# Optimization experiments

Hardware: AMD Instinct MI355X
Metric: run time of the kernel (lower is better)

The kernel has to match this reference:

```python
import jax, jax.numpy as jnp
import numpy as np

N, E, D = 100000, 1600000, 128
EPS = 1e-5


def _bn(h, g, b):
    m = h.mean(0)
    v = ((h - m) ** 2).mean(0)  # biased var, as torch BatchNorm1d normalization
    return g * (h - m) / jnp.sqrt(v + EPS) + b


def _sage(x, src, dst, w_self, w_neigh, b, n):
    # mean aggregation over in-neighbors (edges src->dst)
    agg = jax.ops.segment_sum(x[src], dst, num_segments=n)          # [N, D]
    cnt = jax.ops.segment_sum(jnp.ones(src.shape, x.dtype), dst, num_segments=n)
    mean = agg / jnp.maximum(cnt, 1.0)[:, None]
    return x @ w_self + mean @ w_neigh + b


def setup_inputs() -> dict:
    key = jax.random.key(0)
    ks = jax.random.split(key, 8)
    s = 1.0 / np.sqrt(D)
    return {
        "x": jax.random.normal(ks[0], (N, D), jnp.float32),
        "src": jax.random.randint(ks[1], (E,), 0, N, jnp.int32),
        "dst": jax.random.randint(ks[2], (E,), 0, N, jnp.int32),
        "w_self1": jax.random.normal(ks[3], (D, D), jnp.float32) * s,
        "w_neigh1": jax.random.normal(ks[4], (D, D), jnp.float32) * s,
        "b1": jnp.zeros((D,), jnp.float32),
        "w_self2": jax.random.normal(ks[5], (D, D), jnp.float32) * s,
        "w_neigh2": jax.random.normal(ks[6], (D, D), jnp.float32) * s,
        "b2": jnp.zeros((D,), jnp.float32),
        "w_skip": jax.random.normal(ks[7], (D, D), jnp.float32) * s,
        "b_skip": jnp.zeros((D,), jnp.float32),
        "g1": jnp.ones((D,), jnp.float32), "be1": jnp.zeros((D,), jnp.float32),
        "g2": jnp.ones((D,), jnp.float32), "be2": jnp.zeros((D,), jnp.float32),
        "g3": jnp.ones((D,), jnp.float32), "be3": jnp.zeros((D,), jnp.float32),
    }


def reference(x, src, dst, w_self1, w_neigh1, b1, w_self2, w_neigh2, b2,
              w_skip, b_skip, g1, be1, g2, be2, g3, be3):
    n = x.shape[0]
    h1 = _sage(x, src, dst, w_self1, w_neigh1, b1, n)
    h1 = jax.nn.relu(_bn(h1, g1, be1))           # dropout: eval-mode identity
    h2 = _sage(h1, src, dst, w_self2, w_neigh2, b2, n)
    h2 = _bn(h2, g2, be2)
    skip = _bn(h1 @ w_skip + b_skip, g3, be3)
    return jax.nn.relu(h2 + skip)
```

## Files before the change

kernel.cpp:

```cpp
#include <hip/hip_runtime.h>

#define D 128
#define PCHUNK 4096
#define SCAP 8192

typedef short bf16x8 __attribute__((ext_vector_type(8)));
typedef float f32x4 __attribute__((ext_vector_type(4)));

__device__ __forceinline__ ushort f2b(float f){
  unsigned u = __builtin_bit_cast(unsigned, f);
  u += 0x7fffu + ((u >> 16) & 1u);
  return (ushort)(u >> 16);
}
__device__ __forceinline__ float b2f(ushort h){
  unsigned u = ((unsigned)h) << 16;
  return __builtin_bit_cast(float, u);
}

__global__ __launch_bounds__(256) void k_p0(const int* __restrict__ dst,
                                            int* __restrict__ bcnt, int E){
  __shared__ int h[512];
  for (int u=threadIdx.x; u<512; u+=256) h[u]=0;
  __syncthreads();
  for (long long i=(long long)blockIdx.x*256+threadIdx.x; i<E; i+=(long long)gridDim.x*256)
    atomicAdd(&h[dst[i]>>8], 1);
  __syncthreads();
  for (int u=threadIdx.x; u<512; u+=256) if (h[u]) atomicAdd(&bcnt[u], h[u]);
}

__global__ void k_bscan(const int* __restrict__ bcnt, int* __restrict__ bbase,
                        int* __restrict__ bcur, int nb, int E){
  __shared__ int sh[1024];
  int t = threadIdx.x;
  int v = (t<nb) ? bcnt[t] : 0;
  sh[t]=v; __syncthreads();
  for (int off=1; off<1024; off<<=1){
    int add = (t>=off)?sh[t-off]:0;
    __syncthreads();
    sh[t]+=add;
    __syncthreads();
  }
  if (t<nb){ int e=sh[t]-v; bbase[t]=e; bcur[t]=e; }
  if (t==nb) bbase[t]=E;
}

__global__ __launch_bounds__(256) void k_part(const int* __restrict__ src,
        const int* __restrict__ dst, int* __restrict__ bcur,
        int2* __restrict__ pairs, int E){
  __shared__ int hist[512], offA[512], offB[512], gbase[512];
  __shared__ int sS[PCHUNK], sD[PCHUNK];
  const int t = threadIdx.x;
  const int base = blockIdx.x * PCHUNK;
  const int cnt = min(PCHUNK, E - base);
  for (int u=t; u<512; u+=256) hist[u]=0;
  __syncthreads();
  int rs[16], rd[16];
  #pragma unroll
  for (int j=0;j<16;j++){
    int li = j*256 + t;
    if (li < cnt){
      rs[j]=src[base+li]; rd[j]=dst[base+li];
      atomicAdd(&hist[rd[j]>>8],1);
    } else { rs[j]=0; rd[j]=-1; }
  }
  __syncthreads();
  int *cur=offA, *nxt=offB;
  for (int u=t; u<512; u+=256) cur[u]=hist[u];
  __syncthreads();
  for (int off=1; off<512; off<<=1){
    for (int u=t; u<512; u+=256) nxt[u] = cur[u] + ((u>=off)?cur[u-off]:0);
    __syncthreads();
    int* tmp=cur; cur=nxt; nxt=tmp;
  }
  for (int u=t; u<512; u+=256) nxt[u] = cur[u]-hist[u];
  __syncthreads();
  #pragma unroll
  for (int j=0;j<16;j++){
    if (j*256+t < cnt){
      int b = rd[j]>>8;
      int p = atomicAdd(&nxt[b],1);
      sS[p]=rs[j]; sD[p]=rd[j];
    }
  }
  __syncthreads();
  for (int u=t; u<512; u+=256){
    int c = hist[u];
    if (c>0) gbase[u] = atomicAdd(&bcur[u], c);
  }
  __syncthreads();
  #pragma unroll
  for (int j=0;j<16;j++){
    int idx = j*256+t;
    if (idx<cnt){
      int d = sD[idx]; int b = d>>8;
      int gpos = gbase[b] + (idx - (cur[b]-hist[b]));
      pairs[gpos] = make_int2(sS[idx], d);
    }
  }
}

__global__ __launch_bounds__(256) void k_sortb(const int2* __restrict__ pairs,
        const int* __restrict__ bbase, int* __restrict__ offs,
        int* __restrict__ slots, int N, int NB){
  __shared__ int nh[256], nc[256], sc[256];
  __shared__ int stage[SCAP];
  const int b = blockIdx.x, t = threadIdx.x;
  const int base = bbase[b];
  const int cnt  = bbase[b+1] - base;
  nh[t]=0; __syncthreads();
  for (int i=t;i<cnt;i+=256) atomicAdd(&nh[pairs[base+i].y & 255],1);
  __syncthreads();
  int v = nh[t];
  sc[t]=v; __syncthreads();
  for (int off=1; off<256; off<<=1){
    int add = (t>=off)?sc[t-off]:0;
    __syncthreads();
    sc[t]+=add;
    __syncthreads();
  }
  int excl = sc[t]-v;
  nc[t]=excl;
  int node = (b<<8)+t;
  if (node<N) offs[node]=base+excl;
  if (b==NB-1 && t==0) offs[N]=bbase[NB];
  __syncthreads();
  if (cnt<=SCAP){
    for (int i=t;i<cnt;i+=256){
      int2 p = pairs[base+i];
      int pos = atomicAdd(&nc[p.y & 255],1);
      stage[pos]=p.x;
    }
    __syncthreads();
    for (int i=t;i<cnt;i+=256) slots[base+i]=stage[i];
  } else {
    for (int i=t;i<cnt;i+=256){
      int2 p = pairs[base+i];
      int pos = atomicAdd(&nc[p.y & 255],1);
      slots[base+pos]=p.x;
    }
  }
}

__global__ __launch_bounds__(256) void k_xcast(const float* __restrict__ x,
                                               ushort* __restrict__ xb, long long n4){
  long long i = (long long)blockIdx.x*256 + threadIdx.x;
  const long long stride = (long long)gridDim.x*256;
  for (; i < n4; i += stride){
    float4 v = reinterpret_cast<const float4*>(x)[i];
    ushort4 o;
    o.x = f2b(v.x); o.y = f2b(v.y); o.z = f2b(v.z); o.w = f2b(v.w);
    reinterpret_cast<ushort4*>(xb)[i] = o;
  }
}

__global__ void k_wt(const float* __restrict__ W, ushort* __restrict__ Wb, int K, int k0){
  int idx = blockIdx.x*256 + threadIdx.x;
  int k = idx >> 7, c = idx & 127;
  Wb[(size_t)c*K + k0 + k] = f2b(W[idx]);
}

__global__ __launch_bounds__(256) void k_gatherb(const ushort* __restrict__ Xb,
        const int* __restrict__ slots, const int* __restrict__ offs,
        ushort* __restrict__ meanb, int N){
  int node = blockIdx.x*4 + (threadIdx.x >> 6);
  int c2 = (threadIdx.x & 63) * 2;
  if (node >= N) return;
  const int beg = offs[node], end = offs[node+1];
  float sx0=0,sy0=0,sx1=0,sy1=0,sx2=0,sy2=0,sx3=0,sy3=0;
  int j = beg;
  while (j < end && (j & 3)){
    unsigned u = *reinterpret_cast<const unsigned*>(&Xb[(size_t)slots[j]*D + c2]);
    sx0 += b2f((ushort)u); sy0 += b2f((ushort)(u>>16));
    ++j;
  }
  const int nfull = (end - j) >> 2;
  const int4* sp = reinterpret_cast<const int4*>(slots + j);

#define G8(ia, ib) { \
    unsigned u0 = *reinterpret_cast<const unsigned*>(&Xb[(size_t)(ia).x*D + c2]); \
    unsigned u1 = *reinterpret_cast<const unsigned*>(&Xb[(size_t)(ia).y*D + c2]); \
    unsigned u2 = *reinterpret_cast<const unsigned*>(&Xb[(size_t)(ia).z*D + c2]); \
    unsigned u3 = *reinterpret_cast<const unsigned*>(&Xb[(size_t)(ia).w*D + c2]); \
    unsigned u4 = *reinterpret_cast<const unsigned*>(&Xb[(size_t)(ib).x*D + c2]); \
    unsigned u5 = *reinterpret_cast<const unsigned*>(&Xb[(size_t)(ib).y*D + c2]); \
    unsigned u6 = *reinterpret_cast<const unsigned*>(&Xb[(size_t)(ib).z*D + c2]); \
    unsigned u7 = *reinterpret_cast<const unsigned*>(&Xb[(size_t)(ib).w*D + c2]); \
    sx0 += b2f((ushort)u0); sy0 += b2f((ushort)(u0>>16)); \
    sx1 += b2f((ushort)u1); sy1 += b2f((ushort)(u1>>16)); \
    sx2 += b2f((ushort)u2); sy2 += b2f((ushort)(u2>>16)); \
    sx3 += b2f((ushort)u3); sy3 += b2f((ushort)(u3>>16)); \
    sx0 += b2f((ushort)u4); sy0 += b2f((ushort)(u4>>16)); \
    sx1 += b2f((ushort)u5); sy1 += b2f((ushort)(u5>>16)); \
    sx2 += b2f((ushort)u6); sy2 += b2f((ushort)(u6>>16)); \
    sx3 += b2f((ushort)u7); sy3 += b2f((ushort)(u7>>16)); }

  int g = 0;
  if (nfull >= 2){
    int4 ia = sp[0], ib = sp[1];
    for (g = 2; g + 2 <= nfull; g += 2){
      int4 na = sp[g], nb = sp[g+1];
      G8(ia, ib);
      ia = na; ib = nb;
    }
    G8(ia, ib);
  }
  if (g < nfull){
    int4 ia = sp[g];
    unsigned u0 = *reinterpret_cast<const unsigned*>(&Xb[(size_t)ia.x*D + c2]);
    unsigned u1 = *reinterpret_cast<const unsigned*>(&Xb[(size_t)ia.y*D + c2]);
    unsigned u2 = *reinterpret_cast<const unsigned*>(&Xb[(size_t)ia.z*D + c2]);
    unsigned u3 = *reinterpret_cast<const unsigned*>(&Xb[(size_t)ia.w*D + c2]);
    sx0 += b2f((ushort)u0); sy0 += b2f((ushort)(u0>>16));
    sx1 += b2f((ushort)u1); sy1 += b2f((ushort)(u1>>16));
    sx2 += b2f((ushort)u2); sy2 += b2f((ushort)(u2>>16));
    sx3 += b2f((ushort)u3); sy3 += b2f((ushort)(u3>>16));
  }
  j += 4*nfull;
  for (; j < end; ++j){
    unsigned u = *reinterpret_cast<const unsigned*>(&Xb[(size_t)slots[j]*D + c2]);
    sx0 += b2f((ushort)u); sy0 += b2f((ushort)(u>>16));
  }
#undef G8
  float deg = (float)(end - beg);
  float rc = deg > 0.f ? 1.0f/deg : 0.f;
  unsigned o = (unsigned)f2b((sx0+sx1+sx2+sx3)*rc)
             | ((unsigned)f2b((sy0+sy1+sy2+sy3)*rc) << 16);
  *reinterpret_cast<unsigned*>(&meanb[(size_t)node*D + c2]) = o;
}

template<bool SKIP>
__global__ __launch_bounds__(256, 2) void k_mfma(
    const ushort* __restrict__ A0, const ushort* __restrict__ A1,
    const ushort* __restrict__ Wb, const ushort* __restrict__ Wk,
    const float* __restrict__ bias, const float* __restrict__ biasK,
    ushort* __restrict__ C, ushort* __restrict__ Ck,
    float* __restrict__ gS, float* __restrict__ gQ,
    float* __restrict__ gSK, float* __restrict__ gQK, int N, int NT)
{
  __shared__ ushort At[2][64][40];
  __shared__ ushort Wt[2][128][40];
  __shared__ ushort Wkt[SKIP ? 2*128*40 : 1];
  __shared__ float shS[128], shQ[128], shSK[SKIP?128:1], shQK[SKIP?128:1];
  const int tid = threadIdx.x;
  if (tid < 128){ shS[tid]=0.f; shQ[tid]=0.f; if (SKIP){ shSK[tid]=0.f; shQK[tid]=0.f; } }
  const int bid = blockIdx.x, gridN = gridDim.x;
  const int lane = tid & 63, wid = tid >> 6;
  const int wr = wid >> 1, wc = wid & 1;
  const int lr = lane & 15, kq = lane >> 4;
  const int srA = tid >> 2, s8A = (tid & 3) * 8;
  const int srW = tid >> 2, s8W = (tid & 3) * 8;

  int4 va0, va1, va2, va3;
  int4 w0a,w0b, w1a,w1b, w2a,w2b, w3a,w3b;
  int4 k0a,k0b, k1a,k1b, k2a,k2b, k3a,k3b;

#define LOADSET(S, GT, TT) { \
    int grow_ = (GT)*64 + srA; if (grow_ >= N) grow_ = N-1; \
    const ushort* As_ = ((TT) >= 4) ? A1 : A0; \
    va##S = *reinterpret_cast<const int4*>(&As_[(size_t)grow_*D + ((TT)&3)*32 + s8A]); \
    w##S##a = *reinterpret_cast<const int4*>(&Wb[(size_t)srW*256 + (TT)*32 + s8W]); \
    w##S##b = *reinterpret_cast<const int4*>(&Wb[(size_t)(srW+64)*256 + (TT)*32 + s8W]); \
    if (SKIP && (TT) < 4){ \
      k##S##a = *reinterpret_cast<const int4*>(&Wk[(size_t)srW*128 + (TT)*32 + s8W]); \
      k##S##b = *reinterpret_cast<const int4*>(&Wk[(size_t)(srW+64)*128 + (TT)*32 + s8W]); \
    } }

#define WRITESET(S, BW, TT) { \
    *reinterpret_cast<int4*>(&At[BW][srA][s8A]) = va##S; \
    *reinterpret_cast<int4*>(&Wt[BW][srW][s8W]) = w##S##a; \
    *reinterpret_cast<int4*>(&Wt[BW][srW+64][s8W]) = w##S##b; \
    if (SKIP && (TT) < 4){ \
      *reinterpret_cast<int4*>(&Wkt[((BW)*128 + srW)*40 + s8W]) = k##S##a; \
      *reinterpret_cast<int4*>(&Wkt[((BW)*128 + srW + 64)*40 + s8W]) = k##S##b; \
    } }

#define PBAR() { asm volatile("s_waitcnt lgkmcnt(0)" ::: "memory"); \
    __builtin_amdgcn_s_barrier(); __builtin_amdgcn_sched_barrier(0); }

#define STEPBODY(BR, WITHK, ...) { \
    bf16x8 af0 = *reinterpret_cast<const bf16x8*>(&At[BR][32*wr + lr][kq*8]); \
    bf16x8 af1 = *reinterpret_cast<const bf16x8*>(&At[BR][32*wr + 16 + lr][kq*8]); \
    bf16x8 bw0 = *reinterpret_cast<const bf16x8*>(&Wt[BR][64*wc + lr][kq*8]); \
    bf16x8 bw1 = *reinterpret_cast<const bf16x8*>(&Wt[BR][64*wc + 16 + lr][kq*8]); \
    bf16x8 bw2 = *reinterpret_cast<const bf16x8*>(&Wt[BR][64*wc + 32 + lr][kq*8]); \
    bf16x8 bw3 = *reinterpret_cast<const bf16x8*>(&Wt[BR][64*wc + 48 + lr][kq*8]); \
    bf16x8 bk0{}, bk1{}, bk2{}, bk3{}; \
    if (SKIP && (WITHK)){ \
      bk0 = *reinterpret_cast<const bf16x8*>(&Wkt[((BR)*128 + 64*wc + lr)*40 + kq*8]); \
      bk1 = *reinterpret_cast<const bf16x8*>(&Wkt[((BR)*128 + 64*wc + 16 + lr)*40 + kq*8]); \
      bk2 = *reinterpret_cast<const bf16x8*>(&Wkt[((BR)*128 + 64*wc + 32 + lr)*40 + kq*8]); \
      bk3 = *reinterpret_cast<const bf16x8*>(&Wkt[((BR)*128 + 64*wc + 48 + lr)*40 + kq*8]); \
    } \
    __VA_ARGS__; \
    acc[0][0] = __builtin_amdgcn_mfma_f32_16x16x32_bf16(af0, bw0, acc[0][0], 0,0,0); \
    acc[0][1] = __builtin_amdgcn_mfma_f32_16x16x32_bf16(af0, bw1, acc[0][1], 0,0,0); \
    acc[0][2] = __builtin_amdgcn_mfma_f32_16x16x32_bf16(af0, bw2, acc[0][2], 0,0,0); \
    acc[0][3] = __builtin_amdgcn_mfma_f32_16x16x32_bf16(af0, bw3, acc[0][3], 0,0,0); \
    acc[1][0] = __builtin_amdgcn_mfma_f32_16x16x32_bf16(af1, bw0, acc[1][0], 0,0,0); \
    acc[1][1] = __builtin_amdgcn_mfma_f32_16x16x32_bf16(af1, bw1, acc[1][1], 0,0,0); \
    acc[1][2] = __builtin_amdgcn_mfma_f32_16x16x32_bf16(af1, bw2, acc[1][2], 0,0,0); \
    acc[1][3] = __builtin_amdgcn_mfma_f32_16x16x32_bf16(af1, bw3, acc[1][3], 0,0,0); \
    if (SKIP && (WITHK)){ \
      accK[0][0] = __builtin_amdgcn_mfma_f32_16x16x32_bf16(af0, bk0, accK[0][0], 0,0,0); \
      accK[0][1] = __builtin_amdgcn_mfma_f32_16x16x32_bf16(af0, bk1, accK[0][1], 0,0,0); \
      accK[0][2] = __builtin_amdgcn_mfma_f32_16x16x32_bf16(af0, bk2, accK[0][2], 0,0,0); \
      accK[0][3] = __builtin_amdgcn_mfma_f32_16x16x32_bf16(af0, bk3, accK[0][3], 0,0,0); \
      accK[1][0] = __builtin_amdgcn_mfma_f32_16x16x32_bf16(af1, bk0, accK[1][0], 0,0,0); \
      accK[1][1] = __builtin_amdgcn_mfma_f32_16x16x32_bf16(af1, bk1, accK[1][1], 0,0,0); \
      accK[1][2] = __builtin_amdgcn_mfma_f32_16x16x32_bf16(af1, bk2, accK[1][2], 0,0,0); \
      accK[1][3] = __builtin_amdgcn_mfma_f32_16x16x32_bf16(af1, bk3, accK[1][3], 0,0,0); \
    } }

  f32x4 acc[2][4], accK[SKIP?2:1][SKIP?4:1];
  #pragma unroll
  for (int m=0;m<2;m++)
    #pragma unroll
    for (int n=0;n<4;n++){
      acc[m][n] = (f32x4){0.f,0.f,0.f,0.f};
      if (SKIP) accK[m][n] = (f32x4){0.f,0.f,0.f,0.f};
    }
  float bs[4]={0,0,0,0}, bq[4]={0,0,0,0}, bsk[4]={0,0,0,0}, bqk[4]={0,0,0,0};
  float bv[4], bkv[4];
  #pragma unroll
  for (int n=0;n<4;n++){
    bv[n] = bias[64*wc + 16*n + lr];
    bkv[n] = SKIP ? biasK[64*wc + 16*n + lr] : 0.f;
  }

  {
    const int t0 = bid;
    LOADSET(0, t0, 0);
    LOADSET(1, t0, 1);
    LOADSET(2, t0, 2);
    LOADSET(3, t0, 3);
    WRITESET(0, 0, 0);
    PBAR();
  }

  for (int tile = bid; tile < NT; tile += gridN){
    const int tnext = tile + gridN;
    const bool hasnext = (tnext < NT);
    STEPBODY(0, 1, LOADSET(0, tile, 4));
    WRITESET(1, 1, 1); PBAR();
    STEPBODY(1, 1, LOADSET(1, tile, 5));
    WRITESET(2, 0, 2); PBAR();
    STEPBODY(0, 1, LOADSET(2, tile, 6));
    WRITESET(3, 1, 3); PBAR();
    STEPBODY(1, 1, LOADSET(3, tile, 7));
    WRITESET(0, 0, 4); PBAR();
    STEPBODY(0, 0, if (hasnext) LOADSET(0, tnext, 0));
    WRITESET(1, 1, 5); PBAR();
    STEPBODY(1, 0, if (hasnext) LOADSET(1, tnext, 1));
    WRITESET(2, 0, 6); PBAR();
    STEPBODY(0, 0, if (hasnext) LOADSET(2, tnext, 2));
    WRITESET(3, 1, 7); PBAR();
    STEPBODY(1, 0, if (hasnext) LOADSET(3, tnext, 3));
    if (hasnext){ WRITESET(0, 0, 0); PBAR(); }

    #pragma unroll
    for (int m=0;m<2;m++){
      #pragma unroll
      for (int r=0;r<4;r++){
        int row = tile*64 + 32*wr + 16*m + kq*4 + r;
        if (row < N){
          #pragma unroll
          for (int n=0;n<4;n++){
            int col = 64*wc + 16*n + lr;
            float v = acc[m][n][r] + bv[n];
            C[(size_t)row*D + col] = f2b(v);
            bs[n] += v; bq[n] += v*v;
            if (SKIP){
              float u = accK[m][n][r] + bkv[n];
              Ck[(size_t)row*D + col] = f2b(u);
              bsk[n] += u; bqk[n] += u*u;
            }
          }
        }
      }
    }
    #pragma unroll
    for (int m=0;m<2;m++)
      #pragma unroll
      for (int n=0;n<4;n++){
        acc[m][n] = (f32x4){0.f,0.f,0.f,0.f};
        if (SKIP) accK[m][n] = (f32x4){0.f,0.f,0.f,0.f};
      }
  }
#undef LOADSET
#undef WRITESET
#undef PBAR
#undef STEPBODY

  #pragma unroll
  for (int n=0;n<4;n++){
    float s = bs[n], q = bq[n];
    s += __shfl_xor(s,16); s += __shfl_xor(s,32);
    q += __shfl_xor(q,16); q += __shfl_xor(q,32);
    if (kq == 0){
      int col = 64*wc + 16*n + lr;
      atomicAdd(&shS[col], s);
      atomicAdd(&shQ[col], q);
    }
    if (SKIP){
      float sk = bsk[n], qk = bqk[n];
      sk += __shfl_xor(sk,16); sk += __shfl_xor(sk,32);
      qk += __shfl_xor(qk,16); qk += __shfl_xor(qk,32);
      if (kq == 0){
        int col = 64*wc + 16*n + lr;
        atomicAdd(&shSK[col], sk);
        atomicAdd(&shQK[col], qk);
      }
    }
  }
  __syncthreads();
  if (tid < 128){
    unsafeAtomicAdd(&gS[tid], shS[tid]);
    unsafeAtomicAdd(&gQ[tid], shQ[tid]);
    if (SKIP){
      unsafeAtomicAdd(&gSK[tid], shSK[tid]);
      unsafeAtomicAdd(&gQK[tid], shQK[tid]);
    }
  }
}

__global__ void k_bnfin(const float* __restrict__ sum, const float* __restrict__ sq,
                        const float* __restrict__ g, const float* __restrict__ be,
                        float* __restrict__ bnA, float* __restrict__ bnB, float invN){
  int c = threadIdx.x;
  float m = sum[c]*invN;
  float v = sq[c]*invN - m*m;
  float a = g[c]*rsqrtf(fmaxf(v, 0.f) + 1e-5f);
  bnA[c] = a;
  bnB[c] = be[c] - m*a;
}

__global__ __launch_bounds__(256) void k_bnrelub(const ushort* __restrict__ hpre,
      ushort* __restrict__ hb,
      const float* __restrict__ A, const float* __restrict__ Bp, long long n4){
  long long i = (long long)blockIdx.x*256 + threadIdx.x;
  const long long stride = (long long)gridDim.x*256;
  for (; i < n4; i += stride){
    int c = ((int)(i & 31)) << 2;
    float4 a = *reinterpret_cast<const float4*>(A + c);
    float4 b = *reinterpret_cast<const float4*>(Bp + c);
    ushort4 hv = reinterpret_cast<const ushort4*>(hpre)[i];
    ushort4 o;
    o.x = f2b(fmaxf(a.x*b2f(hv.x) + b.x, 0.f));
    o.y = f2b(fmaxf(a.y*b2f(hv.y) + b.y, 0.f));
    o.z = f2b(fmaxf(a.z*b2f(hv.z) + b.z, 0.f));
    o.w = f2b(fmaxf(a.w*b2f(hv.w) + b.w, 0.f));
    reinterpret_cast<ushort4*>(hb)[i] = o;
  }
}

__global__ __launch_bounds__(256) void k_final(const ushort* __restrict__ h2,
      const ushort* __restrict__ sk, float* __restrict__ out,
      const float* __restrict__ A2, const float* __restrict__ B2,
      const float* __restrict__ A3, const float* __restrict__ B3, long long n4){
  long long i = (long long)blockIdx.x*256 + threadIdx.x;
  const long long stride = (long long)gridDim.x*256;
  for (; i < n4; i += stride){
    int c = ((int)(i & 31)) << 2;
    float4 a2 = *reinterpret_cast<const float4*>(A2 + c);
    float4 b2 = *reinterpret_cast<const float4*>(B2 + c);
    float4 a3 = *reinterpret_cast<const float4*>(A3 + c);
    float4 b3 = *reinterpret_cast<const float4*>(B3 + c);
    ushort4 h = reinterpret_cast<const ushort4*>(h2)[i];
    ushort4 s = reinterpret_cast<const ushort4*>(sk)[i];
    float4 v;
    v.x = fmaxf(a2.x*b2f(h.x) + b2.x + a3.x*b2f(s.x) + b3.x, 0.f);
    v.y = fmaxf(a2.y*b2f(h.y) + b2.y + a3.y*b2f(s.y) + b3.y, 0.f);
    v.z = fmaxf(a2.z*b2f(h.z) + b2.z + a3.z*b2f(s.z) + b3.z, 0.f);
    v.w = fmaxf(a2.w*b2f(h.w) + b2.w + a3.w*b2f(s.w) + b3.w, 0.f);
    reinterpret_cast<float4*>(out)[i] = v;
  }
}

extern "C" void kernel_launch(void* const* d_in, const int* in_sizes, int n_in,
                              void* d_out, int out_size, void* d_ws, size_t ws_size,
                              hipStream_t stream) {
  const float* x        = (const float*)d_in[0];
  const int*   src      = (const int*)  d_in[1];
  const int*   dst      = (const int*)  d_in[2];
  const float* w_self1  = (const float*)d_in[3];
  const float* w_neigh1 = (const float*)d_in[4];
  const float* b1       = (const float*)d_in[5];
  const float* w_self2  = (const float*)d_in[6];
  const float* w_neigh2 = (const float*)d_in[7];
  const float* b2       = (const float*)d_in[8];
  const float* w_skip   = (const float*)d_in[9];
  const float* b_skip   = (const float*)d_in[10];
  const float* g1       = (const float*)d_in[11];
  const float* be1      = (const float*)d_in[12];
  const float* g2       = (const float*)d_in[13];
  const float* be2      = (const float*)d_in[14];
  const float* g3       = (const float*)d_in[15];
  const float* be3      = (const float*)d_in[16];
  (void)n_in; (void)ws_size;

  const int N = in_sizes[0] / D;
  const int E = in_sizes[1];
  const int NB = (N + 255) >> 8;
  float* out = (float*)d_out;

  char* p = (char*)d_ws;
  const size_t nd2 = (((size_t)N * D * 2) + 255) / 256 * 256;
  ushort* meanb  = (ushort*)p; p += nd2;
  ushort* h1b    = (ushort*)p; p += nd2;
  ushort* hpre_b = (ushort*)p; p += nd2;
  ushort* skip_b = (ushort*)p; p += nd2;
  ushort* Wb1    = (ushort*)p; p += 256*128*2;
  ushort* Wb2    = (ushort*)p; p += 256*128*2;
  ushort* Wb3    = (ushort*)p; p += 128*128*2;
  int*    offs   = (int*)p;   p += (((size_t)(N+1)*4) + 255) / 256 * 256;
  int*    bcnt   = (int*)p;   p += 2304;
  float*  st     = (float*)p; p += 1536*sizeof(float);
  int*    bbase  = (int*)p;   p += 2304;
  int*    bcur   = (int*)p;   p += 2048;
  float *sum1=st,      *sq1=st+128,  *sum2=st+256, *sq2=st+384, *sum3=st+512, *sq3=st+640;
  float *bnA1=st+768,  *bnB1=st+896, *bnA2=st+1024,*bnB2=st+1152,*bnA3=st+1280,*bnB3=st+1408;

  const size_t slpad = (((size_t)E*4) + 255) / 256 * 256;
  const size_t xbpad = (((size_t)N*D*2) + 255) / 256 * 256;
  int*    slots = (int*)d_out;
  ushort* xb    = (ushort*)((char*)d_out + slpad);
  int2*   pairs = (int2*)((char*)d_out + slpad + xbpad);

  hipMemsetAsync(bcnt, 0, 2304 + 1536*sizeof(float), stream);

  const long long n4 = (long long)N * D / 4;

  k_xcast<<<2048, 256, 0, stream>>>(x, xb, n4);
  k_wt<<<64, 256, 0, stream>>>(w_self1,  Wb1, 256, 0);
  k_wt<<<64, 256, 0, stream>>>(w_neigh1, Wb1, 256, 128);
  k_wt<<<64, 256, 0, stream>>>(w_self2,  Wb2, 256, 0);
  k_wt<<<64, 256, 0, stream>>>(w_neigh2, Wb2, 256, 128);
  k_wt<<<64, 256, 0, stream>>>(w_skip,   Wb3, 128, 0);

  k_p0<<<1024, 256, 0, stream>>>(dst, bcnt, E);
  k_bscan<<<1, 1024, 0, stream>>>(bcnt, bbase, bcur, NB, E);
  k_part<<<(E + PCHUNK - 1)/PCHUNK, 256, 0, stream>>>(src, dst, bcur, pairs, E);
  k_sortb<<<NB, 256, 0, stream>>>(pairs, bbase, offs, slots, N, NB);

  const int gablocks = (N + 3) / 4;
  const int NT = (N + 63) / 64;
  const int gpersist = 512;
  const float invN = 1.0f / (float)N;

  k_gatherb<<<gablocks, 256, 0, stream>>>(xb, slots, offs, meanb, N);
  k_mfma<false><<<gpersist, 256, 0, stream>>>(xb, meanb, Wb1, nullptr, b1, nullptr,
                                              hpre_b, nullptr, sum1, sq1, nullptr, nullptr, N, NT);
  k_bnfin<<<1, 128, 0, stream>>>(sum1, sq1, g1, be1, bnA1, bnB1, invN);
  k_bnrelub<<<4096, 256, 0, stream>>>(hpre_b, h1b, bnA1, bnB1, n4);

  k_gatherb<<<gablocks, 256, 0, stream>>>(h1b, slots, offs, meanb, N);

  k_mfma<true><<<gpersist, 256, 0, stream>>>(h1b, meanb, Wb2, Wb3, b2, b_skip,
                                             hpre_b, skip_b, sum2, sq2, sum3, sq3, N, NT);
  k_bnfin<<<1, 128, 0, stream>>>(sum2, sq2, g2, be2, bnA2, bnB2, invN);
  k_bnfin<<<1, 128, 0, stream>>>(sum3, sq3, g3, be3, bnA3, bnB3, invN);

  k_final<<<4096, 256, 0, stream>>>(hpre_b, skip_b, out, bnA2, bnB2, bnA3, bnB3, n4);
}
```

Measured before the change: 315.8 us.

## Pack edge pairs, merge weight casts, fold BN finalize, raise MFMA priority

Edge pairs are packed into a single 32-bit word (24-bit src plus 8-bit local dst), which halves partition write and sort read traffic. The five weight-transpose launches are merged into one. The BN finalize kernels are folded into the elementwise consumers, which recompute scale and shift in shared memory per block, removing three tiny launches. s_setprio is raised around the MFMA bursts so those waves are favoured in scheduling. The packing assumes N fits in 24 bits, and each of the 4096 blocks now repeats the finalize computation.

```diff
diff --git a/kernel.cpp b/kernel.cpp
--- a/kernel.cpp
+++ b/kernel.cpp
@@ -46,7 +46,7 @@
 
 __global__ __launch_bounds__(256) void k_part(const int* __restrict__ src,
         const int* __restrict__ dst, int* __restrict__ bcur,
-        int2* __restrict__ pairs, int E){
+        unsigned* __restrict__ pairs, int E){
   __shared__ int hist[512], offA[512], offB[512], gbase[512];
   __shared__ int sS[PCHUNK], sD[PCHUNK];
   const int t = threadIdx.x;
@@ -94,12 +94,12 @@
     if (idx<cnt){
       int d = sD[idx]; int b = d>>8;
       int gpos = gbase[b] + (idx - (cur[b]-hist[b]));
-      pairs[gpos] = make_int2(sS[idx], d);
-    }
-  }
-}
-
-__global__ __launch_bounds__(256) void k_sortb(const int2* __restrict__ pairs,
+      pairs[gpos] = (unsigned)sS[idx] | ((unsigned)(d & 255) << 24);
+    }
+  }
+}
+
+__global__ __launch_bounds__(256) void k_sortb(const unsigned* __restrict__ pairs,
         const int* __restrict__ bbase, int* __restrict__ offs,
         int* __restrict__ slots, int N, int NB){
   __shared__ int nh[256], nc[256], sc[256];
@@ -108,7 +108,7 @@
   const int base = bbase[b];
   const int cnt  = bbase[b+1] - base;
   nh[t]=0; __syncthreads();
-  for (int i=t;i<cnt;i+=256) atomicAdd(&nh[pairs[base+i].y & 255],1);
+  for (int i=t;i<cnt;i+=256) atomicAdd(&nh[pairs[base+i] >> 24],1);
   __syncthreads();
   int v = nh[t];
   sc[t]=v; __syncthreads();
@@ -126,17 +126,17 @@
   __syncthreads();
   if (cnt<=SCAP){
     for (int i=t;i<cnt;i+=256){
-      int2 p = pairs[base+i];
-      int pos = atomicAdd(&nc[p.y & 255],1);
-      stage[pos]=p.x;
+      unsigned p = pairs[base+i];
+      int pos = atomicAdd(&nc[p >> 24],1);
+      stage[pos]=(int)(p & 0xffffffu);
     }
     __syncthreads();
     for (int i=t;i<cnt;i+=256) slots[base+i]=stage[i];
   } else {
     for (int i=t;i<cnt;i+=256){
-      int2 p = pairs[base+i];
-      int pos = atomicAdd(&nc[p.y & 255],1);
-      slots[base+pos]=p.x;
+      unsigned p = pairs[base+i];
+      int pos = atomicAdd(&nc[p >> 24],1);
+      slots[base+pos]=(int)(p & 0xffffffu);
     }
   }
 }
@@ -153,9 +153,22 @@
   }
 }
 
-__global__ void k_wt(const float* __restrict__ W, ushort* __restrict__ Wb, int K, int k0){
-  int idx = blockIdx.x*256 + threadIdx.x;
-  int k = idx >> 7, c = idx & 127;
+__global__ __launch_bounds__(256) void k_wtall(
+    const float* __restrict__ w_self1, const float* __restrict__ w_neigh1,
+    const float* __restrict__ w_self2, const float* __restrict__ w_neigh2,
+    const float* __restrict__ w_skip,
+    ushort* __restrict__ Wb1, ushort* __restrict__ Wb2, ushort* __restrict__ Wb3){
+  const int grp = blockIdx.x >> 6;
+  const int idx = (blockIdx.x & 63)*256 + threadIdx.x;
+  const int k = idx >> 7, c = idx & 127;
+  const float* W; ushort* Wb; int K, k0;
+  switch (grp){
+    case 0: W=w_self1;  Wb=Wb1; K=256; k0=0;   break;
+    case 1: W=w_neigh1; Wb=Wb1; K=256; k0=128; break;
+    case 2: W=w_self2;  Wb=Wb2; K=256; k0=0;   break;
+    case 3: W=w_neigh2; Wb=Wb2; K=256; k0=128; break;
+    default:W=w_skip;   Wb=Wb3; K=128; k0=0;   break;
+  }
   Wb[(size_t)c*K + k0 + k] = f2b(W[idx]);
 }
 
@@ -292,6 +305,7 @@
       bk3 = *reinterpret_cast<const bf16x8*>(&Wkt[((BR)*128 + 64*wc + 48 + lr)*40 + kq*8]); \
     } \
     __VA_ARGS__; \
+    __builtin_amdgcn_s_setprio(1); \
     acc[0][0] = __builtin_amdgcn_mfma_f32_16x16x32_bf16(af0, bw0, acc[0][0], 0,0,0); \
     acc[0][1] = __builtin_amdgcn_mfma_f32_16x16x32_bf16(af0, bw1, acc[0][1], 0,0,0); \
     acc[0][2] = __builtin_amdgcn_mfma_f32_16x16x32_bf16(af0, bw2, acc[0][2], 0,0,0); \
@@ -309,7 +323,8 @@
       accK[1][1] = __builtin_amdgcn_mfma_f32_16x16x32_bf16(af1, bk1, accK[1][1], 0,0,0); \
       accK[1][2] = __builtin_amdgcn_mfma_f32_16x16x32_bf16(af1, bk2, accK[1][2], 0,0,0); \
       accK[1][3] = __builtin_amdgcn_mfma_f32_16x16x32_bf16(af1, bk3, accK[1][3], 0,0,0); \
-    } }
+    } \
+    __builtin_amdgcn_s_setprio(0); }
 
   f32x4 acc[2][4], accK[SKIP?2:1][SKIP?4:1];
   #pragma unroll
@@ -423,26 +438,27 @@
   }
 }
 
-__global__ void k_bnfin(const float* __restrict__ sum, const float* __restrict__ sq,
-                        const float* __restrict__ g, const float* __restrict__ be,
-                        float* __restrict__ bnA, float* __restrict__ bnB, float invN){
-  int c = threadIdx.x;
-  float m = sum[c]*invN;
-  float v = sq[c]*invN - m*m;
-  float a = g[c]*rsqrtf(fmaxf(v, 0.f) + 1e-5f);
-  bnA[c] = a;
-  bnB[c] = be[c] - m*a;
-}
-
 __global__ __launch_bounds__(256) void k_bnrelub(const ushort* __restrict__ hpre,
       ushort* __restrict__ hb,
-      const float* __restrict__ A, const float* __restrict__ Bp, long long n4){
+      const float* __restrict__ sum, const float* __restrict__ sq,
+      const float* __restrict__ g, const float* __restrict__ be,
+      float invN, long long n4){
+  __shared__ float A[128], B[128];
+  if (threadIdx.x < 128){
+    int c = threadIdx.x;
+    float m = sum[c]*invN;
+    float v = sq[c]*invN - m*m;
+    float a = g[c]*rsqrtf(fmaxf(v, 0.f) + 1e-5f);
+    A[c] = a;
+    B[c] = be[c] - m*a;
+  }
+  __syncthreads();
   long long i = (long long)blockIdx.x*256 + threadIdx.x;
   const long long stride = (long long)gridDim.x*256;
   for (; i < n4; i += stride){
     int c = ((int)(i & 31)) << 2;
     float4 a = *reinterpret_cast<const float4*>(A + c);
-    float4 b = *reinterpret_cast<const float4*>(Bp + c);
+    float4 b = *reinterpret_cast<const float4*>(B + c);
     ushort4 hv = reinterpret_cast<const ushort4*>(hpre)[i];
     ushort4 o;
     o.x = f2b(fmaxf(a.x*b2f(hv.x) + b.x, 0.f));
@@ -455,8 +471,24 @@
 
 __global__ __launch_bounds__(256) void k_final(const ushort* __restrict__ h2,
       const ushort* __restrict__ sk, float* __restrict__ out,
-      const float* __restrict__ A2, const float* __restrict__ B2,
-      const float* __restrict__ A3, const float* __restrict__ B3, long long n4){
+      const float* __restrict__ sum2, const float* __restrict__ sq2,
+      const float* __restrict__ g2, const float* __restrict__ be2,
+      const float* __restrict__ sum3, const float* __restrict__ sq3,
+      const float* __restrict__ g3, const float* __restrict__ be3,
+      float invN, long long n4){
+  __shared__ float A2[128], B2[128], A3[128], B3[128];
+  if (threadIdx.x < 128){
+    int c = threadIdx.x;
+    float m2 = sum2[c]*invN;
+    float v2 = sq2[c]*invN - m2*m2;
+    float a2 = g2[c]*rsqrtf(fmaxf(v2, 0.f) + 1e-5f);
+    A2[c] = a2; B2[c] = be2[c] - m2*a2;
+    float m3 = sum3[c]*invN;
+    float v3 = sq3[c]*invN - m3*m3;
+    float a3 = g3[c]*rsqrtf(fmaxf(v3, 0.f) + 1e-5f);
+    A3[c] = a3; B3[c] = be3[c] - m3*a3;
+  }
+  __syncthreads();
   long long i = (long long)blockIdx.x*256 + threadIdx.x;
   const long long stride = (long long)gridDim.x*256;
   for (; i < n4; i += stride){
@@ -518,24 +550,20 @@
   int*    bbase  = (int*)p;   p += 2304;
   int*    bcur   = (int*)p;   p += 2048;
   float *sum1=st,      *sq1=st+128,  *sum2=st+256, *sq2=st+384, *sum3=st+512, *sq3=st+640;
-  float *bnA1=st+768,  *bnB1=st+896, *bnA2=st+1024,*bnB2=st+1152,*bnA3=st+1280,*bnB3=st+1408;
 
   const size_t slpad = (((size_t)E*4) + 255) / 256 * 256;
   const size_t xbpad = (((size_t)N*D*2) + 255) / 256 * 256;
-  int*    slots = (int*)d_out;
-  ushort* xb    = (ushort*)((char*)d_out + slpad);
-  int2*   pairs = (int2*)((char*)d_out + slpad + xbpad);
+  int*      slots = (int*)d_out;
+  ushort*   xb    = (ushort*)((char*)d_out + slpad);
+  unsigned* pairs = (unsigned*)((char*)d_out + slpad + xbpad);
 
   hipMemsetAsync(bcnt, 0, 2304 + 1536*sizeof(float), stream);
 
   const long long n4 = (long long)N * D / 4;
 
   k_xcast<<<2048, 256, 0, stream>>>(x, xb, n4);
-  k_wt<<<64, 256, 0, stream>>>(w_self1,  Wb1, 256, 0);
-  k_wt<<<64, 256, 0, stream>>>(w_neigh1, Wb1, 256, 128);
-  k_wt<<<64, 256, 0, stream>>>(w_self2,  Wb2, 256, 0);
-  k_wt<<<64, 256, 0, stream>>>(w_neigh2, Wb2, 256, 128);
-  k_wt<<<64, 256, 0, stream>>>(w_skip,   Wb3, 128, 0);
+  k_wtall<<<320, 256, 0, stream>>>(w_self1, w_neigh1, w_self2, w_neigh2, w_skip,
+                                   Wb1, Wb2, Wb3);
 
   k_p0<<<1024, 256, 0, stream>>>(dst, bcnt, E);
   k_bscan<<<1, 1024, 0, stream>>>(bcnt, bbase, bcur, NB, E);
@@ -550,15 +578,13 @@
   k_gatherb<<<gablocks, 256, 0, stream>>>(xb, slots, offs, meanb, N);
   k_mfma<false><<<gpersist, 256, 0, stream>>>(xb, meanb, Wb1, nullptr, b1, nullptr,
                                               hpre_b, nullptr, sum1, sq1, nullptr, nullptr, N, NT);
-  k_bnfin<<<1, 128, 0, stream>>>(sum1, sq1, g1, be1, bnA1, bnB1, invN);
-  k_bnrelub<<<4096, 256, 0, stream>>>(hpre_b, h1b, bnA1, bnB1, n4);
+  k_bnrelub<<<4096, 256, 0, stream>>>(hpre_b, h1b, sum1, sq1, g1, be1, invN, n4);
 
   k_gatherb<<<gablocks, 256, 0, stream>>>(h1b, slots, offs, meanb, N);
 
   k_mfma<true><<<gpersist, 256, 0, stream>>>(h1b, meanb, Wb2, Wb3, b2, b_skip,
                                              hpre_b, skip_b, sum2, sq2, sum3, sq3, N, NT);
-  k_bnfin<<<1, 128, 0, stream>>>(sum2, sq2, g2, be2, bnA2, bnB2, invN);
-  k_bnfin<<<1, 128, 0, stream>>>(sum3, sq3, g3, be3, bnA3, bnB3, invN);
-
-  k_final<<<4096, 256, 0, stream>>>(hpre_b, skip_b, out, bnA2, bnB2, bnA3, bnB3, n4);
-}
+
+  k_final<<<4096, 256, 0, stream>>>(hpre_b, skip_b, out,
+                                    sum2, sq2, g2, be2, sum3, sq3, g3, be3, invN, n4);
+}
```

Measured after the change: 301.3 us. 1.05x faster.
